# Performance work log

Measured on AMD Instinct MI355X. Metric: run time of the kernel, lower is better.

## Reference

```python
import jax, jax.numpy as jnp
import numpy as np

B, V, C, H, W = 4, 4, 20, 240, 320
M, N = 500000, 2000000   # unique voxels, full points
P, D, K = 100000, 64, 1024  # points per batch, proj dim, num_matches
TAU = 0.07
NEG = -1.0e6


def setup_inputs() -> dict:
    key = jax.random.key(0)
    ks = jax.random.split(key, 12)
    cam_3d_F = jax.random.normal(ks[0], (M, C), jnp.float32)
    cam_2d = jax.random.normal(ks[1], (B * V, C, H, W), jnp.float32)
    feat_proj_3d = jax.random.normal(ks[2], (B, P, D), jnp.float32)
    feat_detach_2d = jax.random.normal(ks[3], (B, P, D), jnp.float32)
    feat_proj_2d = jax.random.normal(ks[4], (B, P, D), jnp.float32)
    feat_detach_3d = jax.random.normal(ks[5], (B, P, D), jnp.float32)
    labels_cls_3d = (jax.random.uniform(ks[6], (B, C)) < 0.7).astype(jnp.float32).at[:, 0].set(1.0)
    labels_cls_2d = (jax.random.uniform(ks[7], (B, C)) < 0.7).astype(jnp.float32).at[:, 0].set(1.0)
    inverse_map = jax.random.randint(ks[8], (N,), 0, M)
    batch_idx = jnp.sort(jax.random.randint(ks[9], (N,), 0, B))
    # sample-without-replacement indices (np.random.choice replace=False analogue)
    match_idx_3d = jax.vmap(lambda k: jax.random.permutation(k, P)[:K])(jax.random.split(ks[10], B))
    match_idx_2d = jax.vmap(lambda k: jax.random.permutation(k, P)[:K])(jax.random.split(ks[11], B))
    return {
        "cam_3d_F": cam_3d_F, "cam_2d": cam_2d,
        "feat_proj_3d": feat_proj_3d, "feat_detach_2d": feat_detach_2d,
        "feat_proj_2d": feat_proj_2d, "feat_detach_3d": feat_detach_3d,
        "labels_cls_3d": labels_cls_3d, "labels_cls_2d": labels_cls_2d,
        "inverse_map": inverse_map, "batch_idx": batch_idx,
        "match_idx_3d": match_idx_3d, "match_idx_2d": match_idx_2d,
    }


def _soft_margin(x, y):
    # F.multilabel_soft_margin_loss: mean over classes then batch == overall mean
    return -jnp.mean(y * jax.nn.log_sigmoid(x) + (1.0 - y) * jax.nn.log_sigmoid(-x))


def _cmg_loss(fea_k, fea_q, idx):
    # fea_*: [B,P,D], idx: [B,K] -> InfoNCE with identity targets, summed over batches
    k = jnp.take_along_axis(fea_k, idx[:, :, None], axis=1)  # [B,K,D]
    q = jnp.take_along_axis(fea_q, idx[:, :, None], axis=1)  # [B,K,D]
    def one(kb, qb):
        logits = jnp.einsum('kd,md->km', kb, qb) / TAU  # [K,K]
        return -jnp.mean(jnp.diagonal(jax.nn.log_softmax(logits, axis=1)))
    return jnp.sum(jax.vmap(one)(k, q))


def reference(cam_3d_F, cam_2d, feat_proj_3d, feat_detach_2d, feat_proj_2d,
              feat_detach_3d, labels_cls_3d, labels_cls_2d,
              inverse_map, batch_idx, match_idx_3d, match_idx_2d):
    # ---- multi_class_loss_3d: gather + per-batch segment mean ----
    cam_full = cam_3d_F[inverse_map]                                   # [N,C]
    seg_sum = jax.ops.segment_sum(cam_full, batch_idx, num_segments=B)  # [B,C]
    cnt = jax.ops.segment_sum(jnp.ones((cam_full.shape[0],), cam_full.dtype),
                              batch_idx, num_segments=B)                # [B]
    cls_feat = seg_sum / cnt[:, None]
    loss_cam_3d = _soft_margin(cls_feat, labels_cls_3d)
    lab_full = labels_cls_3d[batch_idx]                                # [N,C]
    result_3d = jax.nn.softmax(cam_full + (1.0 - lab_full) * NEG, axis=1)
    # ---- multi_class_loss_2d ----
    cam2 = cam_2d.reshape(B, V, C, H, W).transpose(0, 2, 3, 4, 1)      # [B,C,H,W,V]
    predict_2d = cam2.mean(axis=(2, 3, 4))                             # mean over V then HxW
    loss_cam_2d = _soft_margin(predict_2d, labels_cls_2d)
    lab2 = labels_cls_2d[:, :, None, None, None]                       # [B,C,1,1,1]
    result_2d = jax.nn.softmax(cam2 + (1.0 - lab2) * NEG, axis=1)
    # ---- CMG contrastive losses (q side detached in the original) ----
    loss_cmg_3d = _cmg_loss(feat_proj_3d, jax.lax.stop_gradient(feat_detach_2d), match_idx_3d)
    loss_cmg_2d = _cmg_loss(feat_proj_2d, jax.lax.stop_gradient(feat_detach_3d), match_idx_2d)
    # warm weights and loss weights all 1.0 (post-warmup)
    loss = loss_cam_3d + loss_cam_2d + loss_cmg_3d + loss_cmg_2d
    return (loss, result_3d, result_2d)
```

## Files before the change

kernel.cpp:

```cpp
#include <hip/hip_runtime.h>

#define FLT_NEG_MAX -3.402823466e38f
#define NEGC -1000000.0f
#define INV_TAU (1.0f/0.07f)

static const long long NN = 2000000LL;

#define WS_KBUF 256
#define WS_PM   (WS_KBUF + 524288)
#define WS_PS   (WS_PM + 131072)
#define WS_DIAG (WS_PS + 131072)

#define NB_A 1792
#define NB_B 4800
#define NB_C 512

__device__ __forceinline__ float wave_sum64(float v) {
  v += __shfl_xor(v, 1, 64);
  v += __shfl_xor(v, 2, 64);
  v += __shfl_xor(v, 4, 64);
  v += __shfl_xor(v, 8, 64);
  v += __shfl_xor(v, 16, 64);
  v += __shfl_xor(v, 32, 64);
  return v;
}
__device__ __forceinline__ float wave_max64(float v) {
  v = fmaxf(v, __shfl_xor(v, 1, 64));
  v = fmaxf(v, __shfl_xor(v, 2, 64));
  v = fmaxf(v, __shfl_xor(v, 4, 64));
  v = fmaxf(v, __shfl_xor(v, 8, 64));
  v = fmaxf(v, __shfl_xor(v, 16, 64));
  v = fmaxf(v, __shfl_xor(v, 32, 64));
  return v;
}
__device__ __forceinline__ float logsig(float x) {
  float z = -x;
  return -(fmaxf(z, 0.0f) + log1pf(__expf(-fabsf(z))));
}

__global__ __launch_bounds__(256) void mega1(const float* __restrict__ cam3d,
                                             const float* __restrict__ lab3_g,
                                             const int* __restrict__ inv_map,
                                             const int* __restrict__ bidx,
                                             float* __restrict__ out_r3,
                                             const float* __restrict__ cam2d,
                                             const float* __restrict__ lab2_g,
                                             float* __restrict__ out_r2,
                                             const float* __restrict__ fp3,
                                             const float* __restrict__ fp2,
                                             const int* __restrict__ mi3,
                                             const int* __restrict__ mi2,
                                             float* __restrict__ kbuf,
                                             float* __restrict__ acc) {
  __shared__ float smem[5540];
  const int tid = threadIdx.x;
  const int bid = blockIdx.x;
  const int wid = tid >> 6, lane = tid & 63;

  if (bid < NB_A) {
    float* lab3 = smem;
    float* bins = smem + 80;
    float* stage = smem + 164;
    if (tid < 80) lab3[tid] = lab3_g[tid];
    if (tid < 84) bins[tid] = 0.0f;
    __syncthreads();

    float racc[20];
    #pragma unroll
    for (int c = 0; c < 20; ++c) racc[c] = 0.0f;
    float rcnt = 0.0f;
    int rb_cur = -1;

    const long long stride = (long long)NB_A * 256LL;
    for (long long base = (long long)bid * 256LL; base < NN; base += stride) {
      long long n = base + tid;
      bool active = (n < NN);
      float x[20];
      int b = 0;
      if (active) {
        int iv = inv_map[n];
        b = bidx[n];
        const float4* rp = reinterpret_cast<const float4*>(cam3d + (long long)iv * 20LL);
        #pragma unroll
        for (int q = 0; q < 5; ++q) {
          float4 t4 = rp[q];
          x[4*q+0] = t4.x; x[4*q+1] = t4.y; x[4*q+2] = t4.z; x[4*q+3] = t4.w;
        }
      } else {
        #pragma unroll
        for (int c = 0; c < 20; ++c) x[c] = 0.0f;
      }
      int b0 = __shfl(b, 0, 64);
      bool uni = __all(active) && __all(b == b0);
      if (uni) {
        if (b0 != rb_cur) {
          if (rb_cur >= 0) {
            #pragma unroll
            for (int c = 0; c < 20; ++c) {
              float v = wave_sum64(racc[c]);
              if (lane == 0) atomicAdd(&bins[rb_cur * 20 + c], v);
              racc[c] = 0.0f;
            }
            if (lane == 0) atomicAdd(&bins[80 + rb_cur], rcnt * 64.0f);
            rcnt = 0.0f;
          }
          rb_cur = b0;
        }
        #pragma unroll
        for (int c = 0; c < 20; ++c) racc[c] += x[c];
        rcnt += 1.0f;
      } else if (active) {
        #pragma unroll
        for (int c = 0; c < 20; ++c) atomicAdd(&bins[b * 20 + c], x[c]);
        atomicAdd(&bins[80 + b], 1.0f);
      }
      if (active) {
        float mx = FLT_NEG_MAX;
        #pragma unroll
        for (int c = 0; c < 20; ++c) {
          x[c] += (1.0f - lab3[b * 20 + c]) * NEGC;
          mx = fmaxf(mx, x[c]);
        }
        float s = 0.0f;
        #pragma unroll
        for (int c = 0; c < 20; ++c) { x[c] = __expf(x[c] - mx); s += x[c]; }
        float is = 1.0f / s;
        #pragma unroll
        for (int c = 0; c < 20; ++c) x[c] *= is;
      }
      __syncthreads();
      #pragma unroll
      for (int c = 0; c < 20; ++c) stage[wid * 1344 + lane * 21 + c] = x[c];
      __syncthreads();
      long long nw = base + (long long)wid * 64LL;
      long long rem = NN - nw;
      int valid = rem >= 64 ? 64 : (rem > 0 ? (int)rem : 0);
      if (valid > 0) {
        int lim = valid * 20;
        #pragma unroll
        for (int j = 0; j < 20; ++j) {
          int idx = lane + 64 * j;
          if (idx < lim) {
            int rl = idx / 20;
            int cc = idx - rl * 20;
            __builtin_nontemporal_store(stage[wid * 1344 + rl * 21 + cc],
                                        &out_r3[nw * 20LL + idx]);
          }
        }
      }
    }
    if (rb_cur >= 0) {
      #pragma unroll
      for (int c = 0; c < 20; ++c) {
        float v = wave_sum64(racc[c]);
        if (lane == 0) atomicAdd(&bins[rb_cur * 20 + c], v);
      }
      if (lane == 0) atomicAdd(&bins[80 + rb_cur], rcnt * 64.0f);
    }
    __syncthreads();
    if (tid < 84) atomicAdd(&acc[tid], bins[tid]);

  } else if (bid < NB_A + NB_B) {
    const int rb = bid - NB_A;
    const int b = rb / 1200;
    const int rem = rb - b * 1200;
    const int h = rem / 5;
    const int wt = rem - h * 5;
    const int wl = tid >> 2, v = tid & 3;
    const int w = wt * 64 + wl;
    float* bins2 = smem;
    if (tid < 20) bins2[tid] = 0.0f;
    __syncthreads();
    const float* inb = cam2d + ((long long)(b * 4 + v) * 20LL) * 76800LL
                     + (long long)h * 320 + w;
    float x[20];
    #pragma unroll
    for (int c = 0; c < 20; ++c) x[c] = inb[(long long)c * 76800LL];
    #pragma unroll
    for (int c = 0; c < 20; ++c) {
      float s = wave_sum64(x[c]);
      if (lane == 0) atomicAdd(&bins2[c], s);
    }
    float mx = FLT_NEG_MAX;
    #pragma unroll
    for (int c = 0; c < 20; ++c) {
      x[c] += (1.0f - lab2_g[b * 20 + c]) * NEGC;
      mx = fmaxf(mx, x[c]);
    }
    float s = 0.0f;
    #pragma unroll
    for (int c = 0; c < 20; ++c) { x[c] = __expf(x[c] - mx); s += x[c]; }
    float is = 1.0f / s;
    #pragma unroll
    for (int c = 0; c < 20; ++c)
      __builtin_nontemporal_store(x[c] * is,
          &out_r2[(((long long)(b * 20 + c) * 240 + h) * 320 + w) * 4 + v]);
    __syncthreads();
    if (tid < 20) atomicAdd(&acc[84 + b * 20 + tid], bins2[tid]);

  } else {
    int g = (bid - NB_A - NB_B) * 256 + tid;
    int row = g >> 4;
    int d4 = g & 15;
    int pair = row >> 10;
    int l = pair >> 2, b = pair & 3;
    int i = row & 1023;
    int idx = l ? mi2[b * 1024 + i] : mi3[b * 1024 + i];
    const float* src = l ? fp2 : fp3;
    const float4* s4 = reinterpret_cast<const float4*>(src + ((long long)b * 100000 + idx) * 64LL);
    reinterpret_cast<float4*>(kbuf)[(long long)row * 16 + d4] = s4[d4];
  }
}

__global__ __launch_bounds__(256) void kD(const float* __restrict__ kbuf,
                                          const float* __restrict__ fd2,
                                          const float* __restrict__ fd3,
                                          const int* __restrict__ mi3,
                                          const int* __restrict__ mi2,
                                          float* __restrict__ pm,
                                          float* __restrict__ ps,
                                          float* __restrict__ diag) {
  const int wglob = blockIdx.x * 4 + (threadIdx.x >> 6);
  const int lane = threadIdx.x & 63;
  const int pair = wglob >> 9;
  const int cb = (wglob >> 5) & 15;
  const int rb = wglob & 31;
  const int l = pair >> 2, b = pair & 3;
  const int colg = cb * 64 + lane;
  const int qi = l ? mi2[b * 1024 + colg] : mi3[b * 1024 + colg];
  const float* fq = l ? fd3 : fd2;
  const float4* q4 = reinterpret_cast<const float4*>(fq + ((long long)b * 100000 + qi) * 64LL);
  float4 q[16];
  #pragma unroll
  for (int d = 0; d < 16; ++d) q[d] = q4[d];
  const float* kbase = kbuf + ((long long)pair * 1024 + rb * 32) * 64LL;
  float m_keep = 0.0f, s_keep = 0.0f;
  for (int r = 0; r < 32; ++r) {
    const float4* kr = reinterpret_cast<const float4*>(kbase + r * 64);
    float a0 = 0, a1 = 0, a2 = 0, a3 = 0;
    #pragma unroll
    for (int d = 0; d < 16; ++d) {
      float4 kv = kr[d];
      a0 = fmaf(kv.x, q[d].x, a0);
      a1 = fmaf(kv.y, q[d].y, a1);
      a2 = fmaf(kv.z, q[d].z, a2);
      a3 = fmaf(kv.w, q[d].w, a3);
    }
    float vlog = (a0 + a1 + a2 + a3) * INV_TAU;
    int rowg = rb * 32 + r;
    if (colg == rowg) diag[pair * 1024 + rowg] = vlog;
    float mx = wave_max64(vlog);
    float se = wave_sum64(__expf(vlog - mx));
    if (lane == r) { m_keep = mx; s_keep = se; }
  }
  if (lane < 32) {
    int off = (pair * 16 + cb) * 1024 + rb * 32 + lane;
    pm[off] = m_keep;
    ps[off] = s_keep;
  }
}

__global__ __launch_bounds__(256) void kE(const float* __restrict__ pm,
                                          const float* __restrict__ ps,
                                          const float* __restrict__ diag,
                                          float* __restrict__ acc) {
  const int row = blockIdx.x * 256 + threadIdx.x;
  const int pair = row >> 10;
  const int rl = row & 1023;
  const int l = pair >> 2;
  float m = FLT_NEG_MAX, s = 0.0f;
  #pragma unroll
  for (int cb = 0; cb < 16; ++cb) {
    float mm = pm[(pair * 16 + cb) * 1024 + rl];
    float ss = ps[(pair * 16 + cb) * 1024 + rl];
    if (mm > m) { s = s * __expf(m - mm) + ss; m = mm; }
    else        { s += ss * __expf(mm - m); }
  }
  float r = diag[row] - (m + __logf(s));
  float t = wave_sum64(r);
  __shared__ float wsum[4];
  if ((threadIdx.x & 63) == 0) wsum[threadIdx.x >> 6] = t;
  __syncthreads();
  if (threadIdx.x == 0)
    atomicAdd(&acc[164 + l], wsum[0] + wsum[1] + wsum[2] + wsum[3]);
}

__global__ __launch_bounds__(256) void kF(const float* __restrict__ acc,
                                          const float* __restrict__ lab3,
                                          const float* __restrict__ lab2,
                                          float* __restrict__ out_loss) {
  const int t = threadIdx.x;
  float term = 0.0f;
  if (t < 80) {
    int b = t / 20;
    float x = acc[t] / acc[80 + b];
    float y = lab3[t];
    term = y * logsig(x) + (1.0f - y) * logsig(-x);
  } else if (t < 160) {
    int i = t - 80;
    float x = acc[84 + i] * (1.0f / 307200.0f);
    float y = lab2[i];
    term = y * logsig(x) + (1.0f - y) * logsig(-x);
  }
  float tsum = wave_sum64(term);
  __shared__ float wsum[4];
  if ((t & 63) == 0) wsum[t >> 6] = tsum;
  __syncthreads();
  if (t == 0) {
    float total = wsum[0] + wsum[1] + wsum[2] + wsum[3];
    float margin = -total / 80.0f;
    float cmg = -(acc[164] + acc[165]) / 1024.0f;
    out_loss[0] = margin + cmg;
  }
}

extern "C" void kernel_launch(void* const* d_in, const int* in_sizes, int n_in,
                              void* d_out, int out_size, void* d_ws, size_t ws_size,
                              hipStream_t stream) {
  (void)in_sizes; (void)n_in; (void)out_size; (void)ws_size;
  const float* cam3d = (const float*)d_in[0];
  const float* cam2d = (const float*)d_in[1];
  const float* fp3   = (const float*)d_in[2];
  const float* fd2   = (const float*)d_in[3];
  const float* fp2   = (const float*)d_in[4];
  const float* fd3   = (const float*)d_in[5];
  const float* lab3  = (const float*)d_in[6];
  const float* lab2  = (const float*)d_in[7];
  const int* invm    = (const int*)d_in[8];
  const int* bidx    = (const int*)d_in[9];
  const int* mi3     = (const int*)d_in[10];
  const int* mi2     = (const int*)d_in[11];

  float* out      = (float*)d_out;
  float* out_loss = out;
  float* out_r3   = out + 1;
  float* out_r2   = out + 1 + 40000000LL;

  float* acc  = (float*)d_ws;
  float* kbuf = acc + WS_KBUF;
  float* pm   = acc + WS_PM;
  float* psb  = acc + WS_PS;
  float* diag = acc + WS_DIAG;

  hipMemsetAsync(d_ws, 0, 1024, stream);

  mega1<<<NB_A + NB_B + NB_C, 256, 0, stream>>>(cam3d, lab3, invm, bidx, out_r3,
                                                cam2d, lab2, out_r2,
                                                fp3, fp2, mi3, mi2, kbuf, acc);
  kD<<<1024, 256, 0, stream>>>(kbuf, fd2, fd3, mi3, mi2, pm, psb, diag);
  kE<<<32, 256, 0, stream>>>(pm, psb, diag, acc);
  kF<<<1, 256, 0, stream>>>(acc, lab3, lab2, out_loss);
}
```

Before: 689.6 us.

## Replace grid-stride 3D CAM loop with one tile per block, interleaved with 2D blocks

The persistent grid-stride loop over the 2M points is replaced with one 256-point tile per block, using 7813 blocks. These blocks are interleaved by block index with the 2D CAM and key-gather blocks, so the different memory-bound workloads run at the same time across CUs. The goal is to remove the per-iteration barriers and loop overhead and to spread the load more evenly. In exchange, every block now flushes its 84 partial sums with global atomics to the same few addresses, which adds heavy atomic contention, and the per-wave register accumulation across iterations is lost.

Measured after the change: 739.8 us. 1.07x slower.

```diff
diff --git a/kernel.cpp b/kernel.cpp
--- a/kernel.cpp
+++ b/kernel.cpp
@@ -11,9 +11,10 @@
 #define WS_PS   (WS_PM + 131072)
 #define WS_DIAG (WS_PS + 131072)
 
-#define NB_A 1792
+#define NB_A 7813
+#define NB_BC 5312
+#define NB_T 13125
 #define NB_B 4800
-#define NB_C 512
 
 __device__ __forceinline__ float wave_sum64(float v) {
   v += __shfl_xor(v, 1, 64);
@@ -57,7 +58,12 @@
   const int bid = blockIdx.x;
   const int wid = tid >> 6, lane = tid & 63;
 
-  if (bid < NB_A) {
+  const long long lo = ((long long)bid * NB_A) / NB_T;
+  const bool isA = (((long long)(bid + 1) * NB_A) / NB_T) > lo;
+  const int aid = (int)lo;
+  const int cid = bid - (int)lo;
+
+  if (isA) {
     float* lab3 = smem;
     float* bins = smem + 80;
     float* stage = smem + 164;
@@ -65,103 +71,69 @@
     if (tid < 84) bins[tid] = 0.0f;
     __syncthreads();
 
-    float racc[20];
-    #pragma unroll
-    for (int c = 0; c < 20; ++c) racc[c] = 0.0f;
-    float rcnt = 0.0f;
-    int rb_cur = -1;
-
-    const long long stride = (long long)NB_A * 256LL;
-    for (long long base = (long long)bid * 256LL; base < NN; base += stride) {
-      long long n = base + tid;
-      bool active = (n < NN);
-      float x[20];
-      int b = 0;
-      if (active) {
-        int iv = inv_map[n];
-        b = bidx[n];
-        const float4* rp = reinterpret_cast<const float4*>(cam3d + (long long)iv * 20LL);
-        #pragma unroll
-        for (int q = 0; q < 5; ++q) {
-          float4 t4 = rp[q];
-          x[4*q+0] = t4.x; x[4*q+1] = t4.y; x[4*q+2] = t4.z; x[4*q+3] = t4.w;
-        }
-      } else {
-        #pragma unroll
-        for (int c = 0; c < 20; ++c) x[c] = 0.0f;
+    const long long n = (long long)aid * 256LL + tid;
+    const bool active = (n < NN);
+    float x[20];
+    int b = 0;
+    if (active) {
+      int iv = inv_map[n];
+      b = bidx[n];
+      const float4* rp = reinterpret_cast<const float4*>(cam3d + (long long)iv * 20LL);
+      #pragma unroll
+      for (int q = 0; q < 5; ++q) {
+        float4 t4 = rp[q];
+        x[4*q+0] = t4.x; x[4*q+1] = t4.y; x[4*q+2] = t4.z; x[4*q+3] = t4.w;
       }
-      int b0 = __shfl(b, 0, 64);
-      bool uni = __all(active) && __all(b == b0);
-      if (uni) {
-        if (b0 != rb_cur) {
-          if (rb_cur >= 0) {
-            #pragma unroll
-            for (int c = 0; c < 20; ++c) {
-              float v = wave_sum64(racc[c]);
-              if (lane == 0) atomicAdd(&bins[rb_cur * 20 + c], v);
-              racc[c] = 0.0f;
-            }
-            if (lane == 0) atomicAdd(&bins[80 + rb_cur], rcnt * 64.0f);
-            rcnt = 0.0f;
-          }
-          rb_cur = b0;
-        }
-        #pragma unroll
-        for (int c = 0; c < 20; ++c) racc[c] += x[c];
-        rcnt += 1.0f;
-      } else if (active) {
-        #pragma unroll
-        for (int c = 0; c < 20; ++c) atomicAdd(&bins[b * 20 + c], x[c]);
-        atomicAdd(&bins[80 + b], 1.0f);
+    } else {
+      #pragma unroll
+      for (int c = 0; c < 20; ++c) x[c] = 0.0f;
+    }
+    int b0 = __shfl(b, 0, 64);
+    bool uni = __all(active) && __all(b == b0);
+    if (uni) {
+      #pragma unroll
+      for (int c = 0; c < 20; ++c) {
+        float v = wave_sum64(x[c]);
+        if (lane == 0) atomicAdd(&bins[b0 * 20 + c], v);
       }
-      if (active) {
-        float mx = FLT_NEG_MAX;
-        #pragma unroll
-        for (int c = 0; c < 20; ++c) {
-          x[c] += (1.0f - lab3[b * 20 + c]) * NEGC;
-          mx = fmaxf(mx, x[c]);
-        }
-        float s = 0.0f;
-        #pragma unroll
-        for (int c = 0; c < 20; ++c) { x[c] = __expf(x[c] - mx); s += x[c]; }
-        float is = 1.0f / s;
-        #pragma unroll
-        for (int c = 0; c < 20; ++c) x[c] *= is;
+      if (lane == 0) atomicAdd(&bins[80 + b0], 64.0f);
+    } else if (active) {
+      #pragma unroll
+      for (int c = 0; c < 20; ++c) atomicAdd(&bins[b * 20 + c], x[c]);
+      atomicAdd(&bins[80 + b], 1.0f);
+    }
+    if (active) {
+      float mx = FLT_NEG_MAX;
+      #pragma unroll
+      for (int c = 0; c < 20; ++c) {
+        x[c] += (1.0f - lab3[b * 20 + c]) * NEGC;
+        mx = fmaxf(mx, x[c]);
       }
-      __syncthreads();
-      #pragma unroll
-      for (int c = 0; c < 20; ++c) stage[wid * 1344 + lane * 21 + c] = x[c];
-      __syncthreads();
-      long long nw = base + (long long)wid * 64LL;
-      long long rem = NN - nw;
-      int valid = rem >= 64 ? 64 : (rem > 0 ? (int)rem : 0);
-      if (valid > 0) {
-        int lim = valid * 20;
-        #pragma unroll
-        for (int j = 0; j < 20; ++j) {
-          int idx = lane + 64 * j;
-          if (idx < lim) {
-            int rl = idx / 20;
-            int cc = idx - rl * 20;
-            __builtin_nontemporal_store(stage[wid * 1344 + rl * 21 + cc],
-                                        &out_r3[nw * 20LL + idx]);
-          }
-        }
+      float s = 0.0f;
+      #pragma unroll
+      for (int c = 0; c < 20; ++c) { x[c] = __expf(x[c] - mx); s += x[c]; }
+      float is = 1.0f / s;
+      #pragma unroll
+      for (int c = 0; c < 20; ++c) x[c] *= is;
+    }
+    #pragma unroll
+    for (int c = 0; c < 20; ++c) stage[wid * 1344 + lane * 21 + c] = x[c];
+    __syncthreads();
+    if (active) {
+      const long long nw = (long long)aid * 256LL + (long long)wid * 64LL;
+      #pragma unroll
+      for (int j = 0; j < 20; ++j) {
+        int idx = lane + 64 * j;
+        int rl = idx / 20;
+        int cc = idx - rl * 20;
+        __builtin_nontemporal_store(stage[wid * 1344 + rl * 21 + cc],
+                                    &out_r3[nw * 20LL + idx]);
       }
     }
-    if (rb_cur >= 0) {
-      #pragma unroll
-      for (int c = 0; c < 20; ++c) {
-        float v = wave_sum64(racc[c]);
-        if (lane == 0) atomicAdd(&bins[rb_cur * 20 + c], v);
-      }
-      if (lane == 0) atomicAdd(&bins[80 + rb_cur], rcnt * 64.0f);
-    }
-    __syncthreads();
     if (tid < 84) atomicAdd(&acc[tid], bins[tid]);
 
-  } else if (bid < NB_A + NB_B) {
-    const int rb = bid - NB_A;
+  } else if (cid < NB_B) {
+    const int rb = cid;
     const int b = rb / 1200;
     const int rem = rb - b * 1200;
     const int h = rem / 5;
@@ -199,7 +171,7 @@
     if (tid < 20) atomicAdd(&acc[84 + b * 20 + tid], bins2[tid]);
 
   } else {
-    int g = (bid - NB_A - NB_B) * 256 + tid;
+    int g = (cid - NB_B) * 256 + tid;
     int row = g >> 4;
     int d4 = g & 15;
     int pair = row >> 10;
@@ -344,9 +316,9 @@
 
   hipMemsetAsync(d_ws, 0, 1024, stream);
 
-  mega1<<<NB_A + NB_B + NB_C, 256, 0, stream>>>(cam3d, lab3, invm, bidx, out_r3,
-                                                cam2d, lab2, out_r2,
-                                                fp3, fp2, mi3, mi2, kbuf, acc);
+  mega1<<<NB_T, 256, 0, stream>>>(cam3d, lab3, invm, bidx, out_r3,
+                                  cam2d, lab2, out_r2,
+                                  fp3, fp2, mi3, mi2, kbuf, acc);
   kD<<<1024, 256, 0, stream>>>(kbuf, fd2, fd3, mi3, mi2, pm, psb, diag);
   kE<<<32, 256, 0, stream>>>(pm, psb, diag, acc);
   kF<<<1, 256, 0, stream>>>(acc, lab3, lab2, out_loss);
```
